# Optimization experiments

Measured on AMD Instinct MI355X. Metric: run time of the kernel, lower is better.

The kernel has to match this reference:

```python
import jax, jax.numpy as jnp
import numpy as np

B, V, C, M, CM, D, OUT = 16, 16, 64, 32, 16, 128, 600
VOCAB = {"cond": 4000, "proc": 2000, "drug": 600, "lab_item": 700, "lab_value": 2000, "inj_item": 400, "inj_value": 2000}


def _gru(x, Wih, Whh, bih, bhh):
    """Batch-first torch-style GRU. x: [N,T,D] -> (outputs [N,T,D], h_T [N,D])."""
    Dh = Whh.shape[1]

    def step(h, xt):
        gi = xt @ Wih.T + bih
        gh = h @ Whh.T + bhh
        ir, iz, ig = jnp.split(gi, 3, axis=-1)
        hr, hz, hg = jnp.split(gh, 3, axis=-1)
        r = jax.nn.sigmoid(ir + hr)
        z = jax.nn.sigmoid(iz + hz)
        n = jnp.tanh(ig + r * hg)
        h = (1.0 - z) * n + z * h
        return h, h

    h0 = jnp.zeros((x.shape[0], Dh), x.dtype)
    hT, ys = jax.lax.scan(step, h0, jnp.swapaxes(x, 0, 1))
    return jnp.swapaxes(ys, 0, 1), hT


def _hetero_mp(feats, Wself, Wmsg):
    """Heterogeneous message passing over node types on the fully-connected
    monitor<->visit-feature bipartite pattern: each node type combines a self
    transform with a transformed mean of the other node types, then ReLU.
    feats: list of [N,D]; Wself/Wmsg: [T,D,D]."""
    stacked = jnp.stack(feats)  # [T,N,D]
    total = jnp.sum(stacked, axis=0)
    T = stacked.shape[0]
    outs = []
    for t in range(T):
        others = (total - stacked[t]) / (T - 1)
        outs.append(jax.nn.relu(stacked[t] @ Wself[t] + others @ Wmsg[t]))
    return outs


def _forward(codes_cond, codes_proc, codes_drug, codes_lab_item, codes_lab_value,
             codes_inj_item, codes_inj_value, weight, age,
             emb_cond, emb_proc, emb_drug, emb_lab_item, emb_lab_value,
             emb_inj_item, emb_inj_value,
             mgru_Wih, mgru_Whh, mgru_bih, mgru_bhh,
             vgru_Wih, vgru_Whh, vgru_bih, vgru_bhh,
             gnn_Wself, gnn_Wmsg,
             fc_weight_W, fc_weight_b, fc_age_W, fc_age_b,
             fc_patient_W, fc_patient_b):
    # ---- visit-event features: embedding lookup + sum-pool over codes ----
    vis = {}
    for k, codes, emb in (("cond", codes_cond, emb_cond),
                          ("proc", codes_proc, emb_proc),
                          ("drug", codes_drug, emb_drug)):
        vis[k] = jnp.sum(emb[codes], axis=2)  # [B,V,D]
    visit_keys = ("cond", "proc", "drug")

    # ---- monitor-event pairs: (item * value) embeddings, GNN, two-level GRU ----
    pairs = (
        (codes_lab_item, codes_lab_value, emb_lab_item, emb_lab_value, "lab_item", (0, 2, 3, 4)),
        (codes_inj_item, codes_inj_value, emb_inj_item, emb_inj_value, "inj_item", (1, 2, 3, 4)),
    )
    hid = {}
    for p, (ci, cv, ei, ev, ikey, gidx) in enumerate(pairs):
        mon = jnp.sum(ei[ci] * ev[cv], axis=3)  # [B,V,M,D]
        feats = [mon.reshape(-1, D)]  # monitor node type, [B*V*M, D]
        for k in visit_keys:  # visit features repeated across monitors
            feats.append(jnp.broadcast_to(vis[k][:, :, None, :], (B, V, M, D)).reshape(-1, D))
        outs = _hetero_mp(feats, gnn_Wself[p], gnn_Wmsg[p])
        for t, k in enumerate((ikey,) + visit_keys):
            g = gidx[t]
            # monitor-level GRU over the M monitors of each visit
            o, _ = _gru(outs[t].reshape(B * V, M, D), mgru_Wih[g], mgru_Whh[g], mgru_bih[g], mgru_bhh[g])
            last = o[:, -1, :].reshape(B, V, D)  # last monitor state per visit
            # visit-level GRU (source uses visit_gru[feature_key1] for all keys)
            _, h = _gru(last, vgru_Wih[p], vgru_Whh[p], vgru_bih[p], vgru_bhh[p])
            hid[k] = h if k not in hid else hid[k] + h

    # ---- weight / age scalar features ----
    for k, x, W, b, vi in (("weight", weight, fc_weight_W, fc_weight_b, 2),
                           ("age", age, fc_age_W, fc_age_b, 3)):
        mask = (x != 0.0)[..., None]  # [B,V,1]
        xe = (x[..., None] * W[:, 0] + b) * mask  # Linear(1->D) then zero-mask
        _, h = _gru(xe, vgru_Wih[vi], vgru_Whh[vi], vgru_bih[vi], vgru_bhh[vi])
        hid[k] = h

    # ---- concat in dict-insertion order, then ReLU + Linear head ----
    pe = jnp.concatenate([hid["lab_item"], hid["cond"], hid["proc"], hid["drug"],
                          hid["inj_item"], hid["weight"], hid["age"]], axis=-1)  # [B, 7D]
    return jax.nn.relu(pe) @ fc_patient_W.T + fc_patient_b  # [B, OUT]


def setup_inputs() -> dict:
    key = jax.random.key(0)
    ks = iter(jax.random.split(key, 64))

    def nrm(shape, s=0.1):
        return (jax.random.normal(next(ks), shape) * s).astype(jnp.float32)

    def emb_table(vsz):
        t = nrm((vsz, D), 1.0)
        return t.at[0].set(0.0)  # padding_idx=0 row is zero

    inp = {}
    inp["codes_cond"] = jax.random.randint(next(ks), (B, V, C), 0, VOCAB["cond"], dtype=jnp.int32)
    inp["codes_proc"] = jax.random.randint(next(ks), (B, V, C), 0, VOCAB["proc"], dtype=jnp.int32)
    inp["codes_drug"] = jax.random.randint(next(ks), (B, V, C), 0, VOCAB["drug"], dtype=jnp.int32)
    inp["codes_lab_item"] = jax.random.randint(next(ks), (B, V, M, CM), 0, VOCAB["lab_item"], dtype=jnp.int32)
    inp["codes_lab_value"] = jax.random.randint(next(ks), (B, V, M, CM), 0, VOCAB["lab_value"], dtype=jnp.int32)
    inp["codes_inj_item"] = jax.random.randint(next(ks), (B, V, M, CM), 0, VOCAB["inj_item"], dtype=jnp.int32)
    inp["codes_inj_value"] = jax.random.randint(next(ks), (B, V, M, CM), 0, VOCAB["inj_value"], dtype=jnp.int32)
    inp["weight"] = jax.random.uniform(next(ks), (B, V), minval=0.1, maxval=1.0, dtype=jnp.float32)
    inp["age"] = jax.random.uniform(next(ks), (B, V), minval=0.1, maxval=1.0, dtype=jnp.float32)
    inp["emb_cond"] = emb_table(VOCAB["cond"])
    inp["emb_proc"] = emb_table(VOCAB["proc"])
    inp["emb_drug"] = emb_table(VOCAB["drug"])
    inp["emb_lab_item"] = emb_table(VOCAB["lab_item"])
    inp["emb_lab_value"] = emb_table(VOCAB["lab_value"])
    inp["emb_inj_item"] = emb_table(VOCAB["inj_item"])
    inp["emb_inj_value"] = emb_table(VOCAB["inj_value"])
    inp["mgru_Wih"] = nrm((5, 3 * D, D))
    inp["mgru_Whh"] = nrm((5, 3 * D, D))
    inp["mgru_bih"] = nrm((5, 3 * D))
    inp["mgru_bhh"] = nrm((5, 3 * D))
    inp["vgru_Wih"] = nrm((4, 3 * D, D))
    inp["vgru_Whh"] = nrm((4, 3 * D, D))
    inp["vgru_bih"] = nrm((4, 3 * D))
    inp["vgru_bhh"] = nrm((4, 3 * D))
    inp["gnn_Wself"] = nrm((2, 4, D, D))
    inp["gnn_Wmsg"] = nrm((2, 4, D, D))
    inp["fc_weight_W"] = nrm((D, 1))
    inp["fc_weight_b"] = nrm((D,))
    inp["fc_age_W"] = nrm((D, 1))
    inp["fc_age_b"] = nrm((D,))
    inp["fc_patient_W"] = nrm((OUT, 7 * D))
    inp["fc_patient_b"] = nrm((OUT,))
    return inp


def reference(codes_cond, codes_proc, codes_drug, codes_lab_item, codes_lab_value,
              codes_inj_item, codes_inj_value, weight, age,
              emb_cond, emb_proc, emb_drug, emb_lab_item, emb_lab_value,
              emb_inj_item, emb_inj_value,
              mgru_Wih, mgru_Whh, mgru_bih, mgru_bhh,
              vgru_Wih, vgru_Whh, vgru_bih, vgru_bhh,
              gnn_Wself, gnn_Wmsg,
              fc_weight_W, fc_weight_b, fc_age_W, fc_age_b,
              fc_patient_W, fc_patient_b):
    return _forward(codes_cond, codes_proc, codes_drug, codes_lab_item, codes_lab_value,
                    codes_inj_item, codes_inj_value, weight, age,
                    emb_cond, emb_proc, emb_drug, emb_lab_item, emb_lab_value,
                    emb_inj_item, emb_inj_value,
                    mgru_Wih, mgru_Whh, mgru_bih, mgru_bhh,
                    vgru_Wih, vgru_Whh, vgru_bih, vgru_bhh,
                    gnn_Wself, gnn_Wmsg,
                    fc_weight_W, fc_weight_b, fc_age_W, fc_age_b,
                    fc_patient_W, fc_patient_b)
```

## Files before the change

### kernel.cpp

```cpp
#include <hip/hip_runtime.h>
#include <math.h>

#define B_   16
#define V_   16
#define C_   64
#define M_   32
#define CM_  16
#define D_   128
#define OUT_ 600
#define NSEQ 256
#define NROW 8192

typedef __attribute__((ext_vector_type(8))) short bf16x8;
typedef __attribute__((ext_vector_type(4))) short bf16x4;
typedef __attribute__((ext_vector_type(4))) float f32x4;

__device__ __forceinline__ unsigned short f2bf(float x) {
  union { float f; unsigned u; } v; v.f = x;
  unsigned r = v.u + 0x7fff + ((v.u >> 16) & 1);
  return (unsigned short)(r >> 16);
}
__device__ __forceinline__ float bf2f(short s) {
  union { unsigned u; float f; } v;
  v.u = ((unsigned)(unsigned short)s) << 16;
  return v.f;
}
__device__ __forceinline__ float fsig(float x)  { return __fdividef(1.f, 1.f + __expf(-x)); }
__device__ __forceinline__ float ftanh(float x) { return 1.f - 2.f*__fdividef(1.f, __expf(2.f*x) + 1.f); }

__device__ __forceinline__ void ldsbar() {
  asm volatile("s_waitcnt lgkmcnt(0)" ::: "memory");
  __builtin_amdgcn_s_barrier();
  asm volatile("" ::: "memory");
}

constexpr int OFF_VIS   = 0;
constexpr int OFF_VISB  = 98304;
constexpr int OFF_MONB  = 147456;
constexpr int OFF_TOTB  = 1196032;
constexpr int OFF_W12T  = 2244608;
constexpr int OFF_WIHB  = 2375680;
constexpr int OFF_WIHTV = 2498560;
constexpr int OFF_XE    = 2695168;
constexpr int OFF_LAST  = 27926528;
constexpr int OFF_VH    = 29171712;

__global__ __launch_bounds__(256) void k_prepvis(
    const float* __restrict__ Wself, const float* __restrict__ Wmsg,
    const float* __restrict__ mWih,  const float* __restrict__ vWih,
    const float* __restrict__ wgt,   const float* __restrict__ age,
    const float* __restrict__ fwW,   const float* __restrict__ fwB,
    const float* __restrict__ faW,   const float* __restrict__ faB,
    const int* __restrict__ cc, const int* __restrict__ cp, const int* __restrict__ cd,
    const float* __restrict__ ec, const float* __restrict__ ep, const float* __restrict__ ed,
    short* __restrict__ w12t, short* __restrict__ wihb,
    float* __restrict__ wihTv, float* __restrict__ xe,
    float* __restrict__ vis, short* __restrict__ visb)
{
  int bx = blockIdx.x, tid = threadIdx.x;
  if (bx < 1024) {
    int lin = bx*256 + tid;
    int pt = lin >> 15, rem = lin & 32767;
    int n = rem >> 8, k = rem & 255;
    float v;
    if (k < 128) v = Wself[pt*16384 + k*128 + n] - Wmsg[pt*16384 + k*128 + n]*(1.f/3.f);
    else         v = Wmsg[pt*16384 + (k-128)*128 + n]*(1.f/3.f);
    w12t[lin] = (short)f2bf(v);
  } else if (bx < 1984) {
    int lin = (bx-1024)*256 + tid;
    wihb[lin] = (short)f2bf(mWih[lin]);
  } else if (bx < 2752) {
    int lin = (bx-1984)*256 + tid;
    int g = lin / 49152, rem2 = lin % 49152;
    int k = rem2 / 384, j = rem2 % 384;
    wihTv[lin] = vWih[g*49152 + j*128 + k];
  } else if (bx < 3008) {
    int lin = (bx-2752)*256 + tid;
    int which = lin >> 15, rem2 = lin & 32767;
    int n = rem2 >> 7, d = rem2 & 127;
    float x  = which ? age[n] : wgt[n];
    float Wv = which ? faW[d] : fwW[d];
    float bb = which ? faB[d] : fwB[d];
    xe[lin] = (x != 0.0f) ? (x*Wv + bb) : 0.0f;
  } else {
    int idx = (bx-3008)*256 + tid;
    int type = idx >> 15;
    int r = idx & 32767;
    int bv = r >> 7, d = r & 127;
    const int*   codes = (type==0) ? cc : (type==1) ? cp : cd;
    const float* emb   = (type==0) ? ec : (type==1) ? ep : ed;
    float acc = 0.f;
    for (int c = 0; c < C_; ++c) {
      int code = codes[bv*C_ + c];
      acc += emb[code*D_ + d];
    }
    vis [(type*NSEQ + bv)*D_ + d] = acc;
    visb[(type*NSEQ + bv)*D_ + d] = (short)f2bf(acc);
  }
}

__global__ __launch_bounds__(128) void k_mon(
    const int* __restrict__ cli, const int* __restrict__ clv,
    const int* __restrict__ cii, const int* __restrict__ civ,
    const float* __restrict__ eli, const float* __restrict__ elv,
    const float* __restrict__ eii, const float* __restrict__ eiv,
    const float* __restrict__ vis,
    short* __restrict__ monb, short* __restrict__ totb)
{
  int p   = blockIdx.x >> 13;
  int bvm = blockIdx.x & 8191;
  int d   = threadIdx.x;
  const int* ci = p ? cii : cli;  const int* cv = p ? civ : clv;
  const float* ei = p ? eii : eli; const float* ev = p ? eiv : elv;
  float acc = 0.f;
  #pragma unroll
  for (int c = 0; c < CM_; ++c) {
    int iv = ci[bvm*CM_ + c];
    int vv = cv[bvm*CM_ + c];
    acc += ei[iv*D_ + d] * ev[vv*D_ + d];
  }
  int bv = bvm >> 5;
  float vsum = vis[bv*D_ + d] + vis[(NSEQ + bv)*D_ + d] + vis[(2*NSEQ + bv)*D_ + d];
  monb[(p*NROW + bvm)*D_ + d] = (short)f2bf(acc);
  totb[(p*NROW + bvm)*D_ + d] = (short)f2bf(acc + vsum);
}

__global__ __launch_bounds__(512, 1) void k_ggru(
    const short* __restrict__ monb, const short* __restrict__ totb,
    const short* __restrict__ visb, const short* __restrict__ w12t,
    const short* __restrict__ wihb, const float* __restrict__ mWhh,
    const float* __restrict__ mbih, const float* __restrict__ mbhh,
    float* __restrict__ last)
{
  const int run  = blockIdx.x >> 4;
  const int pair = blockIdx.x & 15;
  const int p = run >> 2, t = run & 3;
  const int g = (run % 4 == 0) ? (run / 4) : (run % 4 + 1);
  const int tid = threadIdx.x;
  const int w = tid >> 6;
  const int lane = tid & 63;
  const int c = lane & 15, q = lane >> 4;
  const int j = w*16 + c;

  __shared__ short hb[2][4][16][40];
  __shared__ __align__(16) short Ys[16][136];
  __shared__ __align__(16) short Xl[2][4096];

  for (int idx = tid; idx < 2*4*16*40; idx += 512)
    ((short*)hb)[idx] = 0;

  bf16x8 bW12[8];
  #pragma unroll
  for (int kt = 0; kt < 8; ++kt)
    bW12[kt] = *(const bf16x8*)(w12t + (size_t)run*32768 + (size_t)(w*16+c)*256 + kt*32 + q*8);

  bf16x8 bWih[3][4];
  #pragma unroll
  for (int gate = 0; gate < 3; ++gate)
    #pragma unroll
    for (int kt = 0; kt < 4; ++kt)
      bWih[gate][kt] = *(const bf16x8*)(wihb + ((size_t)g*384 + gate*128 + j)*128 + kt*32 + q*8);

  bf16x8 bWhh[3][4];
  #pragma unroll
  for (int gate = 0; gate < 3; ++gate) {
    const float* wp = mWhh + ((size_t)g*384 + gate*128 + j)*128 + q*8;
    #pragma unroll
    for (int kt = 0; kt < 4; ++kt) {
      float4 lo = *(const float4*)(wp + kt*32);
      float4 hi = *(const float4*)(wp + kt*32 + 4);
      bf16x8 tt;
      tt[0]=(short)f2bf(lo.x); tt[1]=(short)f2bf(lo.y); tt[2]=(short)f2bf(lo.z); tt[3]=(short)f2bf(lo.w);
      tt[4]=(short)f2bf(hi.x); tt[5]=(short)f2bf(hi.y); tt[6]=(short)f2bf(hi.z); tt[7]=(short)f2bf(hi.w);
      bWhh[gate][kt] = tt;
    }
  }
  const float bs0 = mbih[g*384 +       j] + mbhh[g*384 +       j];
  const float bs1 = mbih[g*384 + 128 + j] + mbhh[g*384 + 128 + j];
  const float bi2 = mbih[g*384 + 256 + j];
  const float bh2 = mbhh[g*384 + 256 + j];

  const int xr_ = tid >> 5, xu = tid & 31;
  const int bv = pair*16 + xr_;
  const short* fsrc;
  int fstride;
  if (xu < 16) {
    if (t == 0) { fsrc = monb + ((size_t)p*NROW + (size_t)bv*32)*128 + xu*8; fstride = 128; }
    else        { fsrc = visb + ((size_t)(t-1)*NSEQ + bv)*128 + xu*8;        fstride = 0;   }
  } else {
    fsrc = totb + ((size_t)p*NROW + (size_t)bv*32)*128 + (xu-16)*8;          fstride = 128;
  }
  const int xdofs = xr_*256 + (((xu*16) ^ ((xr_&7)<<4)) >> 1);
  short* xdst0 = &Xl[0][xdofs];
  short* xdst1 = &Xl[1][xdofs];

  {
    bf16x8 x0 = *(const bf16x8*)fsrc;
    *(bf16x8*)xdst0 = x0;
  }
  float hf[4] = {0.f,0.f,0.f,0.f};
  const int ktw = w >> 1;
  const int kkw = (w & 1)*16 + c;
  ldsbar();

  #pragma unroll 1
  for (int m = 0; m < 32; ++m) {
    const int cur = m & 1;
    bf16x8 xnext;
    if (m < 31) xnext = *(const bf16x8*)(fsrc + (size_t)(m+1)*fstride);

    const char* xbase = (const char*)&Xl[cur][0];
    f32x4 accY = (f32x4){0.f,0.f,0.f,0.f};
    #pragma unroll
    for (int kt = 0; kt < 8; ++kt) {
      bf16x8 aX = *(const bf16x8*)(xbase + c*512 + ((kt*64 + q*16) ^ ((c&7)<<4)));
      accY = __builtin_amdgcn_mfma_f32_16x16x32_bf16(aX, bW12[kt], accY, 0, 0, 0);
    }
    #pragma unroll
    for (int reg = 0; reg < 4; ++reg)
      Ys[q*4 + reg][w*16 + c] = (short)f2bf(fmaxf(accY[reg], 0.f));
    ldsbar();

    bf16x8 ah[4], a2[4];
    #pragma unroll
    for (int kt = 0; kt < 4; ++kt) {
      ah[kt] = *(const bf16x8*)&hb[cur][kt][c][q*8];
      a2[kt] = *(const bf16x8*)&Ys[c][kt*32 + q*8];
    }
    f32x4 acc0 = (f32x4){0.f,0.f,0.f,0.f};
    f32x4 acc1 = (f32x4){0.f,0.f,0.f,0.f};
    f32x4 aG2  = (f32x4){0.f,0.f,0.f,0.f};
    f32x4 aH2  = (f32x4){0.f,0.f,0.f,0.f};
    #pragma unroll
    for (int kt = 0; kt < 4; ++kt) {
      acc0 = __builtin_amdgcn_mfma_f32_16x16x32_bf16(ah[kt], bWhh[0][kt], acc0, 0, 0, 0);
      acc1 = __builtin_amdgcn_mfma_f32_16x16x32_bf16(ah[kt], bWhh[1][kt], acc1, 0, 0, 0);
      aH2  = __builtin_amdgcn_mfma_f32_16x16x32_bf16(ah[kt], bWhh[2][kt], aH2,  0, 0, 0);
    }
    #pragma unroll
    for (int kt = 0; kt < 4; ++kt) {
      acc0 = __builtin_amdgcn_mfma_f32_16x16x32_bf16(a2[kt], bWih[0][kt], acc0, 0, 0, 0);
      acc1 = __builtin_amdgcn_mfma_f32_16x16x32_bf16(a2[kt], bWih[1][kt], acc1, 0, 0, 0);
      aG2  = __builtin_amdgcn_mfma_f32_16x16x32_bf16(a2[kt], bWih[2][kt], aG2,  0, 0, 0);
    }

    if (m < 31) *(bf16x8*)(cur ? xdst0 : xdst1) = xnext;

    const int nxt = cur ^ 1;
    #pragma unroll
    for (int reg = 0; reg < 4; ++reg) {
      float rr = fsig(acc0[reg] + bs0);
      float zz = fsig(acc1[reg] + bs1);
      float nn = ftanh(aG2[reg] + bi2 + rr*(aH2[reg] + bh2));
      float hnew = (1.f - zz)*nn + zz*hf[reg];
      hf[reg] = hnew;
      hb[nxt][ktw][q*4 + reg][kkw] = (short)f2bf(hnew);
    }
    ldsbar();
  }

  #pragma unroll
  for (int reg = 0; reg < 4; ++reg)
    last[((size_t)run*NSEQ + pair*16 + q*4 + reg)*D_ + j] = hf[reg];
}

__global__ __launch_bounds__(768) void k_vgru(
    const float* __restrict__ last, const float* __restrict__ xe,
    const float* __restrict__ wihTv, const float* __restrict__ vbih,
    const float* __restrict__ vWhh, const float* __restrict__ vbhh,
    float* __restrict__ vh)
{
  int run = blockIdx.x >> 4, b = blockIdx.x & 15;
  int tid = threadIdx.x;
  int vidx = (run < 4) ? 0 : (run < 8) ? 1 : (run - 6);

  __shared__ float Xs[16][128];
  __shared__ float giL[16*384];
  __shared__ __align__(16) float hsv[128];
  __shared__ float gh[384];

  const float* X = (run < 8) ? (last + ((size_t)run*NSEQ + b*16)*D_)
                             : (xe + ((size_t)(run-8)*NSEQ + b*16)*D_);
  for (int idx = tid; idx < 2048; idx += 768)
    ((float*)Xs)[idx] = X[idx];
  if (tid < 128) hsv[tid] = 0.f;
  __syncthreads();

  {
    int half = (tid >= 384) ? 1 : 0;
    int j = tid - half*384;
    float accv[8];
    float bias = vbih[vidx*384 + j];
    #pragma unroll
    for (int s = 0; s < 8; ++s) accv[s] = bias;
    const float* W = wihTv + vidx*49152 + j;
    #pragma unroll 4
    for (int k = 0; k < 128; ++k) {
      float wv = W[k*384];
      #pragma unroll
      for (int s = 0; s < 8; ++s) accv[s] += Xs[half*8 + s][k] * wv;
    }
    #pragma unroll
    for (int s = 0; s < 8; ++s)
      giL[(half*8 + s)*384 + j] = accv[s];
  }

  int j = tid >> 1, kh = tid & 1;
  float w[64];
  const float4* wrow = (const float4*)(vWhh + (vidx*384 + j)*128 + kh*64);
  #pragma unroll
  for (int k4 = 0; k4 < 16; ++k4) {
    float4 t4 = wrow[k4];
    w[4*k4] = t4.x; w[4*k4+1] = t4.y; w[4*k4+2] = t4.z; w[4*k4+3] = t4.w;
  }
  float bj = vbhh[vidx*384 + j];
  __syncthreads();

  #pragma unroll 1
  for (int v = 0; v < 16; ++v) {
    const float4* h4 = (const float4*)(hsv + kh*64);
    float p0 = 0.f, p1 = 0.f;
    #pragma unroll
    for (int k4 = 0; k4 < 8; ++k4) {
      float4 u0 = h4[k4], u1 = h4[k4+8];
      p0 += w[4*k4   ]*u0.x + w[4*k4+1 ]*u0.y + w[4*k4+2 ]*u0.z + w[4*k4+3 ]*u0.w;
      p1 += w[4*k4+32]*u1.x + w[4*k4+33]*u1.y + w[4*k4+34]*u1.z + w[4*k4+35]*u1.w;
    }
    float part = p0 + p1;
    part += __shfl_xor(part, 1);
    if (kh == 0) gh[j] = bj + ((j < 256) ? giL[v*384 + j] : 0.f) + part;
    __syncthreads();
    if (tid < 128) {
      float r = fsig(gh[tid]);
      float z = fsig(gh[tid+128]);
      float gin = giL[v*384 + 256 + tid];
      float n = ftanh(gin + r*gh[tid+256]);
      hsv[tid] = (1.f - z)*n + z*hsv[tid];
    }
    __syncthreads();
  }
  if (tid < 128) vh[(run*16 + b)*D_ + tid] = hsv[tid];
}

__global__ __launch_bounds__(256) void k_head(
    const float* __restrict__ vh, const float* __restrict__ Wp,
    const float* __restrict__ bp, float* __restrict__ out)
{
  const int o = blockIdx.x;
  const int tid = threadIdx.x;
  const int b = tid & 15, kc = tid >> 4;
  const int a1[7] = {0,1,2,3,4,8,9};
  const int a2[7] = {-1,5,6,7,-1,-1,-1};
  const float4* wb = (const float4*)(Wp + (size_t)o*896 + kc*56);
  float acc = 0.f;
  #pragma unroll
  for (int i = 0; i < 14; ++i) {
    int cc2 = kc*56 + i*4;
    int s = cc2 >> 7, d0 = cc2 & 127;
    float4 a = *(const float4*)(vh + (a1[s]*16 + b)*D_ + d0);
    int s2 = a2[s];
    if (s2 >= 0) {
      float4 a2v = *(const float4*)(vh + (s2*16 + b)*D_ + d0);
      a.x += a2v.x; a.y += a2v.y; a.z += a2v.z; a.w += a2v.w;
    }
    a.x = fmaxf(a.x, 0.f); a.y = fmaxf(a.y, 0.f);
    a.z = fmaxf(a.z, 0.f); a.w = fmaxf(a.w, 0.f);
    float4 ww = wb[i];
    acc += a.x*ww.x + a.y*ww.y + a.z*ww.z + a.w*ww.w;
  }
  __shared__ float red[16][17];
  red[kc][b] = acc;
  __syncthreads();
  if (tid < 16) {
    float s = 0.f;
    #pragma unroll
    for (int k = 0; k < 16; ++k) s += red[k][tid];
    out[tid*OUT_ + o] = s + bp[o];
  }
}

extern "C" void kernel_launch(void* const* d_in, const int* in_sizes, int n_in,
                              void* d_out, int out_size, void* d_ws, size_t ws_size,
                              hipStream_t stream)
{
  (void)in_sizes; (void)n_in; (void)out_size; (void)ws_size;
  const int*   cc   = (const int*)  d_in[0];
  const int*   cp   = (const int*)  d_in[1];
  const int*   cd   = (const int*)  d_in[2];
  const int*   cli  = (const int*)  d_in[3];
  const int*   clv  = (const int*)  d_in[4];
  const int*   cii  = (const int*)  d_in[5];
  const int*   civ  = (const int*)  d_in[6];
  const float* wgt  = (const float*)d_in[7];
  const float* age  = (const float*)d_in[8];
  const float* ec   = (const float*)d_in[9];
  const float* ep   = (const float*)d_in[10];
  const float* ed   = (const float*)d_in[11];
  const float* eli  = (const float*)d_in[12];
  const float* elv  = (const float*)d_in[13];
  const float* eii  = (const float*)d_in[14];
  const float* eiv  = (const float*)d_in[15];
  const float* mWih = (const float*)d_in[16];
  const float* mWhh = (const float*)d_in[17];
  const float* mbih = (const float*)d_in[18];
  const float* mbhh = (const float*)d_in[19];
  const float* vWih = (const float*)d_in[20];
  const float* vWhh = (const float*)d_in[21];
  const float* vbih = (const float*)d_in[22];
  const float* vbhh = (const float*)d_in[23];
  const float* Wself= (const float*)d_in[24];
  const float* Wmsg = (const float*)d_in[25];
  const float* fwW  = (const float*)d_in[26];
  const float* fwB  = (const float*)d_in[27];
  const float* faW  = (const float*)d_in[28];
  const float* faB  = (const float*)d_in[29];
  const float* Wp   = (const float*)d_in[30];
  const float* bp   = (const float*)d_in[31];
  float* out = (float*)d_out;
  float* ws  = (float*)d_ws;

  float* vis   = ws + OFF_VIS;
  short* visb  = (short*)(ws + OFF_VISB);
  short* monb  = (short*)(ws + OFF_MONB);
  short* totb  = (short*)(ws + OFF_TOTB);
  short* w12t  = (short*)(ws + OFF_W12T);
  short* wihb  = (short*)(ws + OFF_WIHB);
  float* wihTv = ws + OFF_WIHTV;
  float* xe    = ws + OFF_XE;
  float* last  = ws + OFF_LAST;
  float* vh    = ws + OFF_VH;

  k_prepvis<<<3392, 256, 0, stream>>>(Wself, Wmsg, mWih, vWih, wgt, age,
                                      fwW, fwB, faW, faB,
                                      cc, cp, cd, ec, ep, ed,
                                      w12t, wihb, wihTv, xe, vis, visb);
  k_mon <<<16384, 128, 0, stream>>>(cli, clv, cii, civ, eli, elv, eii, eiv,
                                    vis, monb, totb);
  k_ggru<<<128, 512, 0, stream>>>(monb, totb, visb, w12t, wihb,
                                  mWhh, mbih, mbhh, last);
  k_vgru<<<160, 768, 0, stream>>>(last, xe, wihTv, vbih, vWhh, vbhh, vh);
  k_head<<<600, 256, 0, stream>>>(vh, Wp, bp, out);
}
```

Before: 252.0 us.

## Software-pipeline the Y projection one step ahead in the GRU loop

The monitor GRU kernel now computes the ReLU message projection (Y) for step m+1 during step m and double-buffers Ys. This removes one block barrier per timestep and lets the projection MFMAs overlap with the recurrent gate MFMAs. The input prefetch moves two steps ahead to match. In exchange it uses more LDS and adds register pressure from carrying an extra accumulator.

```diff
diff --git a/kernel.cpp b/kernel.cpp
--- a/kernel.cpp
+++ b/kernel.cpp
@@ -143,7 +143,7 @@
   const int j = w*16 + c;
 
   __shared__ short hb[2][4][16][40];
-  __shared__ __align__(16) short Ys[16][136];
+  __shared__ __align__(16) short Ys[2][16][136];
   __shared__ __align__(16) short Xl[2][4096];
 
   for (int idx = tid; idx < 2*4*16*40; idx += 512)
@@ -196,20 +196,17 @@
 
   {
     bf16x8 x0 = *(const bf16x8*)fsrc;
+    bf16x8 x1 = *(const bf16x8*)(fsrc + fstride);
     *(bf16x8*)xdst0 = x0;
+    *(bf16x8*)xdst1 = x1;
   }
   float hf[4] = {0.f,0.f,0.f,0.f};
   const int ktw = w >> 1;
   const int kkw = (w & 1)*16 + c;
   ldsbar();
 
-  #pragma unroll 1
-  for (int m = 0; m < 32; ++m) {
-    const int cur = m & 1;
-    bf16x8 xnext;
-    if (m < 31) xnext = *(const bf16x8*)(fsrc + (size_t)(m+1)*fstride);
-
-    const char* xbase = (const char*)&Xl[cur][0];
+  {
+    const char* xbase = (const char*)&Xl[0][0];
     f32x4 accY = (f32x4){0.f,0.f,0.f,0.f};
     #pragma unroll
     for (int kt = 0; kt < 8; ++kt) {
@@ -218,14 +215,32 @@
     }
     #pragma unroll
     for (int reg = 0; reg < 4; ++reg)
-      Ys[q*4 + reg][w*16 + c] = (short)f2bf(fmaxf(accY[reg], 0.f));
-    ldsbar();
+      Ys[0][q*4 + reg][w*16 + c] = (short)f2bf(fmaxf(accY[reg], 0.f));
+  }
+  ldsbar();
+
+  #pragma unroll 1
+  for (int m = 0; m < 32; ++m) {
+    const int cur = m & 1, nxt = cur ^ 1;
+
+    bf16x8 xnext;
+    if (m < 30) xnext = *(const bf16x8*)(fsrc + (size_t)(m+2)*fstride);
+
+    f32x4 accY = (f32x4){0.f,0.f,0.f,0.f};
+    if (m < 31) {
+      const char* xbase = (const char*)&Xl[nxt][0];
+      #pragma unroll
+      for (int kt = 0; kt < 8; ++kt) {
+        bf16x8 aX = *(const bf16x8*)(xbase + c*512 + ((kt*64 + q*16) ^ ((c&7)<<4)));
+        accY = __builtin_amdgcn_mfma_f32_16x16x32_bf16(aX, bW12[kt], accY, 0, 0, 0);
+      }
+    }
 
     bf16x8 ah[4], a2[4];
     #pragma unroll
     for (int kt = 0; kt < 4; ++kt) {
       ah[kt] = *(const bf16x8*)&hb[cur][kt][c][q*8];
-      a2[kt] = *(const bf16x8*)&Ys[c][kt*32 + q*8];
+      a2[kt] = *(const bf16x8*)&Ys[cur][c][kt*32 + q*8];
     }
     f32x4 acc0 = (f32x4){0.f,0.f,0.f,0.f};
     f32x4 acc1 = (f32x4){0.f,0.f,0.f,0.f};
@@ -244,9 +259,13 @@
       aG2  = __builtin_amdgcn_mfma_f32_16x16x32_bf16(a2[kt], bWih[2][kt], aG2,  0, 0, 0);
     }
 
-    if (m < 31) *(bf16x8*)(cur ? xdst0 : xdst1) = xnext;
-
-    const int nxt = cur ^ 1;
+    if (m < 31) {
+      #pragma unroll
+      for (int reg = 0; reg < 4; ++reg)
+        Ys[nxt][q*4 + reg][w*16 + c] = (short)f2bf(fmaxf(accY[reg], 0.f));
+    }
+    if (m < 30) *(bf16x8*)(cur ? xdst1 : xdst0) = xnext;
+
     #pragma unroll
     for (int reg = 0; reg < 4; ++reg) {
       float rr = fsig(acc0[reg] + bs0);
```

New measurement: 248.2 us. Within noise of the previous version (-1.5%).

## Precompute all GNN message outputs before GRU recurrence with direct-to-register loads

Applied to the files above, without the earlier changes.

Moves the per-step message-passing MFMA (X·W12 with ReLU) out of the sequential GRU loop into a prologue that computes all 32 timesteps into a large LDS buffer. Inputs are loaded straight into registers with inline-asm global_load_dwordx4 and double-buffered with manual vmcnt waits, instead of staging through LDS. The recurrent loop then only reads precomputed Y and uses split accumulators to shorten MFMA dependency chains, removing one barrier per step. The cost is a 128KB LDS footprint and more registers.

```diff
diff --git a/kernel.cpp b/kernel.cpp
--- a/kernel.cpp
+++ b/kernel.cpp
@@ -14,6 +14,7 @@
 typedef __attribute__((ext_vector_type(8))) short bf16x8;
 typedef __attribute__((ext_vector_type(4))) short bf16x4;
 typedef __attribute__((ext_vector_type(4))) float f32x4;
+typedef __attribute__((ext_vector_type(4))) unsigned int u32x4;
 
 __device__ __forceinline__ unsigned short f2bf(float x) {
   union { float f; unsigned u; } v; v.f = x;
@@ -33,6 +34,10 @@
   __builtin_amdgcn_s_barrier();
   asm volatile("" ::: "memory");
 }
+
+#define GLD4(dst, ptr, offstr) \
+  asm volatile("global_load_dwordx4 %0, %1, off offset:" offstr \
+               : "=v"(dst) : "v"(ptr) : "memory")
 
 constexpr int OFF_VIS   = 0;
 constexpr int OFF_VISB  = 98304;
@@ -142,9 +147,8 @@
   const int c = lane & 15, q = lane >> 4;
   const int j = w*16 + c;
 
+  __shared__ short YsAll[32*2048];
   __shared__ short hb[2][4][16][40];
-  __shared__ __align__(16) short Ys[16][136];
-  __shared__ __align__(16) short Xl[2][4096];
 
   for (int idx = tid; idx < 2*4*16*40; idx += 512)
     ((short*)hb)[idx] = 0;
@@ -152,7 +156,61 @@
   bf16x8 bW12[8];
   #pragma unroll
   for (int kt = 0; kt < 8; ++kt)
-    bW12[kt] = *(const bf16x8*)(w12t + (size_t)run*32768 + (size_t)(w*16+c)*256 + kt*32 + q*8);
+    bW12[kt] = *(const bf16x8*)(w12t + (size_t)run*32768 + (size_t)j*256 + kt*32 + q*8);
+
+  const short* fA = (t == 0)
+      ? monb + ((size_t)p*NROW + (size_t)(pair*16 + c)*32)*128 + q*8
+      : visb + ((size_t)(t-1)*NSEQ + pair*16 + c)*128 + q*8;
+  const int fAstride = (t == 0) ? 128 : 0;
+  const short* tA = totb + ((size_t)p*NROW + (size_t)(pair*16 + c)*32)*128 + q*8;
+
+  const short* fp = fA;
+  const short* tp = tA;
+  u32x4 pfA[8], pfB[8];
+
+  auto issue8 = [&](u32x4 (&buf)[8]) {
+    GLD4(buf[0], fp, "0");   GLD4(buf[1], fp, "64");
+    GLD4(buf[2], fp, "128"); GLD4(buf[3], fp, "192");
+    GLD4(buf[4], tp, "0");   GLD4(buf[5], tp, "64");
+    GLD4(buf[6], tp, "128"); GLD4(buf[7], tp, "192");
+    fp += fAstride; tp += 128;
+  };
+  auto computeY = [&](u32x4 (&buf)[8], int m) {
+    f32x4 ya = (f32x4){0.f,0.f,0.f,0.f};
+    f32x4 yb = (f32x4){0.f,0.f,0.f,0.f};
+    #pragma unroll
+    for (int kt = 0; kt < 4; ++kt) {
+      ya = __builtin_amdgcn_mfma_f32_16x16x32_bf16(*(bf16x8*)&buf[kt],   bW12[kt],   ya, 0, 0, 0);
+      yb = __builtin_amdgcn_mfma_f32_16x16x32_bf16(*(bf16x8*)&buf[kt+4], bW12[kt+4], yb, 0, 0, 0);
+    }
+    char* ybase = (char*)YsAll + m*4096;
+    #pragma unroll
+    for (int reg = 0; reg < 4; ++reg) {
+      int srow = q*4 + reg;
+      *(short*)(ybase + srow*256 + ((2*j) ^ ((srow&7)<<4)))
+          = (short)f2bf(fmaxf(ya[reg] + yb[reg], 0.f));
+    }
+  };
+
+  issue8(pfA);
+  #pragma unroll 1
+  for (int m2 = 0; m2 < 15; ++m2) {
+    issue8(pfB);
+    asm volatile("s_waitcnt vmcnt(8)" ::: "memory");
+    __builtin_amdgcn_sched_barrier(0);
+    computeY(pfA, 2*m2);
+    issue8(pfA);
+    asm volatile("s_waitcnt vmcnt(8)" ::: "memory");
+    __builtin_amdgcn_sched_barrier(0);
+    computeY(pfB, 2*m2 + 1);
+  }
+  issue8(pfB);
+  asm volatile("s_waitcnt vmcnt(8)" ::: "memory");
+  __builtin_amdgcn_sched_barrier(0);
+  computeY(pfA, 30);
+  asm volatile("s_waitcnt vmcnt(0)" ::: "memory");
+  __builtin_amdgcn_sched_barrier(0);
+  computeY(pfB, 31);
 
   bf16x8 bWih[3][4];
   #pragma unroll
@@ -180,77 +238,38 @@
   const float bi2 = mbih[g*384 + 256 + j];
   const float bh2 = mbhh[g*384 + 256 + j];
 
-  const int xr_ = tid >> 5, xu = tid & 31;
-  const int bv = pair*16 + xr_;
-  const short* fsrc;
-  int fstride;
-  if (xu < 16) {
-    if (t == 0) { fsrc = monb + ((size_t)p*NROW + (size_t)bv*32)*128 + xu*8; fstride = 128; }
-    else        { fsrc = visb + ((size_t)(t-1)*NSEQ + bv)*128 + xu*8;        fstride = 0;   }
-  } else {
-    fsrc = totb + ((size_t)p*NROW + (size_t)bv*32)*128 + (xu-16)*8;          fstride = 128;
-  }
-  const int xdofs = xr_*256 + (((xu*16) ^ ((xr_&7)<<4)) >> 1);
-  short* xdst0 = &Xl[0][xdofs];
-  short* xdst1 = &Xl[1][xdofs];
-
-  {
-    bf16x8 x0 = *(const bf16x8*)fsrc;
-    *(bf16x8*)xdst0 = x0;
-  }
   float hf[4] = {0.f,0.f,0.f,0.f};
   const int ktw = w >> 1;
   const int kkw = (w & 1)*16 + c;
+
   ldsbar();
 
   #pragma unroll 1
   for (int m = 0; m < 32; ++m) {
-    const int cur = m & 1;
-    bf16x8 xnext;
-    if (m < 31) xnext = *(const bf16x8*)(fsrc + (size_t)(m+1)*fstride);
-
-    const char* xbase = (const char*)&Xl[cur][0];
-    f32x4 accY = (f32x4){0.f,0.f,0.f,0.f};
-    #pragma unroll
-    for (int kt = 0; kt < 8; ++kt) {
-      bf16x8 aX = *(const bf16x8*)(xbase + c*512 + ((kt*64 + q*16) ^ ((c&7)<<4)));
-      accY = __builtin_amdgcn_mfma_f32_16x16x32_bf16(aX, bW12[kt], accY, 0, 0, 0);
-    }
-    #pragma unroll
-    for (int reg = 0; reg < 4; ++reg)
-      Ys[q*4 + reg][w*16 + c] = (short)f2bf(fmaxf(accY[reg], 0.f));
-    ldsbar();
-
+    const int cur = m & 1, nxt = cur ^ 1;
     bf16x8 ah[4], a2[4];
+    const char* yb2 = (const char*)YsAll + m*4096;
     #pragma unroll
     for (int kt = 0; kt < 4; ++kt) {
       ah[kt] = *(const bf16x8*)&hb[cur][kt][c][q*8];
-      a2[kt] = *(const bf16x8*)&Ys[c][kt*32 + q*8];
-    }
-    f32x4 acc0 = (f32x4){0.f,0.f,0.f,0.f};
-    f32x4 acc1 = (f32x4){0.f,0.f,0.f,0.f};
-    f32x4 aG2  = (f32x4){0.f,0.f,0.f,0.f};
-    f32x4 aH2  = (f32x4){0.f,0.f,0.f,0.f};
+      a2[kt] = *(const bf16x8*)(yb2 + c*256 + ((kt*64 + q*16) ^ ((c&7)<<4)));
+    }
+    f32x4 a0a = (f32x4){0.f,0.f,0.f,0.f}, a0b = (f32x4){0.f,0.f,0.f,0.f};
+    f32x4 a1a = (f32x4){0.f,0.f,0.f,0.f}, a1b = (f32x4){0.f,0.f,0.f,0.f};
+    f32x4 aG2 = (f32x4){0.f,0.f,0.f,0.f}, aH2 = (f32x4){0.f,0.f,0.f,0.f};
     #pragma unroll
     for (int kt = 0; kt < 4; ++kt) {
-      acc0 = __builtin_amdgcn_mfma_f32_16x16x32_bf16(ah[kt], bWhh[0][kt], acc0, 0, 0, 0);
-      acc1 = __builtin_amdgcn_mfma_f32_16x16x32_bf16(ah[kt], bWhh[1][kt], acc1, 0, 0, 0);
-      aH2  = __builtin_amdgcn_mfma_f32_16x16x32_bf16(ah[kt], bWhh[2][kt], aH2,  0, 0, 0);
-    }
-    #pragma unroll
-    for (int kt = 0; kt < 4; ++kt) {
-      acc0 = __builtin_amdgcn_mfma_f32_16x16x32_bf16(a2[kt], bWih[0][kt], acc0, 0, 0, 0);
-      acc1 = __builtin_amdgcn_mfma_f32_16x16x32_bf16(a2[kt], bWih[1][kt], acc1, 0, 0, 0);
-      aG2  = __builtin_amdgcn_mfma_f32_16x16x32_bf16(a2[kt], bWih[2][kt], aG2,  0, 0, 0);
-    }
-
-    if (m < 31) *(bf16x8*)(cur ? xdst0 : xdst1) = xnext;
-
-    const int nxt = cur ^ 1;
+      a0a = __builtin_amdgcn_mfma_f32_16x16x32_bf16(ah[kt], bWhh[0][kt], a0a, 0, 0, 0);
+      a0b = __builtin_amdgcn_mfma_f32_16x16x32_bf16(a2[kt], bWih[0][kt], a0b, 0, 0, 0);
+      a1a = __builtin_amdgcn_mfma_f32_16x16x32_bf16(ah[kt], bWhh[1][kt], a1a, 0, 0, 0);
+      a1b = __builtin_amdgcn_mfma_f32_16x16x32_bf16(a2[kt], bWih[1][kt], a1b, 0, 0, 0);
+      aH2 = __builtin_amdgcn_mfma_f32_16x16x32_bf16(ah[kt], bWhh[2][kt], aH2, 0, 0, 0);
+      aG2 = __builtin_amdgcn_mfma_f32_16x16x32_bf16(a2[kt], bWih[2][kt], aG2, 0, 0, 0);
+    }
     #pragma unroll
     for (int reg = 0; reg < 4; ++reg) {
-      float rr = fsig(acc0[reg] + bs0);
-      float zz = fsig(acc1[reg] + bs1);
+      float rr = fsig(a0a[reg] + a0b[reg] + bs0);
+      float zz = fsig(a1a[reg] + a1b[reg] + bs1);
       float nn = ftanh(aG2[reg] + bi2 + rr*(aH2[reg] + bh2));
       float hnew = (1.f - zz)*nn + zz*hf[reg];
       hf[reg] = hnew;
```

Measured after the change: 292.6 us. 1.16x slower.
